# Kernel optimization log

Hardware: AMD Instinct MI355X
Metric: run time of the kernel (lower is better)

Reference implementation:

```python
import jax, jax.numpy as jnp
import numpy as np
from jax import lax

L, B, T = 512, 1024, 48


def setup_inputs() -> dict:
    key = jax.random.key(0)
    k1, k2, k3, k4, k5 = jax.random.split(key, 5)
    emissions = jax.random.normal(k1, (L, B, T), dtype=jnp.float32)
    tags = jax.random.randint(k2, (L, B), 0, T)
    mask = jnp.ones((L, B), dtype=bool)
    start_transitions = jax.random.uniform(k3, (T,), minval=-0.1, maxval=0.1, dtype=jnp.float32)
    end_transitions = jax.random.uniform(k4, (T,), minval=-0.1, maxval=0.1, dtype=jnp.float32)
    transitions = jax.random.uniform(k5, (T, T), minval=-0.1, maxval=0.1, dtype=jnp.float32)
    return {
        'emissions': emissions,
        'tags': tags,
        'mask': mask,
        'start_transitions': start_transitions,
        'end_transitions': end_transitions,
        'transitions': transitions,
    }


def reference(emissions, tags, mask, start_transitions, end_transitions, transitions):
    # emissions: [L, B, T] float; tags: [L, B] int; mask: [L, B] bool (seq-first)
    fm = mask.astype(emissions.dtype)
    seq_len, batch, _ = emissions.shape
    b_idx = jnp.arange(batch)

    # ---- numerator: score of the gold path ----
    # emission score at each step: emissions[i, b, tags[i, b]] -> [L, B]
    em_sc = jnp.take_along_axis(emissions, tags[:, :, None], axis=2)[:, :, 0]
    # transition score between consecutive tags -> [L-1, B]
    trans_sc = transitions[tags[:-1], tags[1:]]
    score = start_transitions[tags[0]] + em_sc[0]
    score = score + jnp.sum((trans_sc + em_sc[1:]) * fm[1:], axis=0)
    seq_ends = mask.astype(jnp.int32).sum(axis=0) - 1  # [B]
    last_tags = tags[seq_ends, b_idx]
    score = score + end_transitions[last_tags]

    # ---- denominator: log partition via forward algorithm (scan) ----
    alpha0 = start_transitions + emissions[0]  # [B, T]

    def step(alpha, xs):
        em, m = xs  # em: [B, T], m: [B]
        # [B, T(prev), T(next)] logsumexp over prev
        next_alpha = jax.nn.logsumexp(
            alpha[:, :, None] + transitions[None, :, :] + em[:, None, :], axis=1)
        alpha = jnp.where(m[:, None], next_alpha, alpha)
        return alpha, None

    alpha, _ = lax.scan(step, alpha0, (emissions[1:], mask[1:]))
    denominator = jax.nn.logsumexp(alpha + end_transitions, axis=1)  # [B]

    llh = score - denominator
    return jnp.mean(llh)  # reduction='mean' (default)
```

## Files before the change

kernel.cpp:

```cpp
#include <hip/hip_runtime.h>

#define LSEQ 512
#define BATCH 1024
#define T 48

__global__ __launch_bounds__(256) void crf_forward(
    const float* __restrict__ emissions,
    const int* __restrict__ mask,
    const float* __restrict__ start_tr,
    const float* __restrict__ end_tr,
    const float* __restrict__ trans,
    float* __restrict__ denom_out)
{
    const int wave = threadIdx.x >> 6;
    const int lane = threadIdx.x & 63;
    const int b    = blockIdx.x * 4 + wave;
    const int j    = lane;
    const bool valid = (j < T);
    const int jc   = valid ? j : (T - 1);

    float E_col[T];
    #pragma unroll
    for (int i = 0; i < T; ++i) {
        E_col[i] = __expf(trans[i * T + jc]);
    }

    float alpha = valid ? (start_tr[jc] + emissions[((size_t)0 * BATCH + b) * T + jc])
                        : -1e30f;

    float em_a = emissions[((size_t)1 * BATCH + b) * T + jc];
    float em_b = emissions[((size_t)2 * BATCH + b) * T + jc];
    int mk_a = mask[1 * BATCH + b];
    int mk_b = mask[2 * BATCH + b];

    for (int t = 1; t < LSEQ; ++t) {
        const float em_t = em_a;  em_a = em_b;
        const int mt = mk_a;  mk_a = mk_b;
        int tn = t + 2; if (tn > LSEQ - 1) tn = LSEQ - 1;
        em_b = emissions[((size_t)tn * BATCH + b) * T + jc];
        mk_b = mask[tn * BATCH + b];

        const float ref = __int_as_float(
            __builtin_amdgcn_readlane(__float_as_int(alpha), 0));
        const float p = __expf(alpha - ref);
        const int pbits = __float_as_int(p);

        float s0 = 0.f, s1 = 0.f, s2 = 0.f, s3 = 0.f;
        #pragma unroll
        for (int i = 0; i < T; i += 4) {
            s0 = __builtin_fmaf(__int_as_float(__builtin_amdgcn_readlane(pbits, i    )), E_col[i    ], s0);
            s1 = __builtin_fmaf(__int_as_float(__builtin_amdgcn_readlane(pbits, i + 1)), E_col[i + 1], s1);
            s2 = __builtin_fmaf(__int_as_float(__builtin_amdgcn_readlane(pbits, i + 2)), E_col[i + 2], s2);
            s3 = __builtin_fmaf(__int_as_float(__builtin_amdgcn_readlane(pbits, i + 3)), E_col[i + 3], s3);
        }
        const float s = (s0 + s1) + (s2 + s3);
        const float anew = em_t + ref + __logf(s);
        if (mt && valid) alpha = anew;
    }

    float v = valid ? (alpha + end_tr[jc]) : -1e30f;
    float m = v;
    #pragma unroll
    for (int off = 32; off > 0; off >>= 1) m = fmaxf(m, __shfl_xor(m, off));
    float e = __expf(v - m);
    #pragma unroll
    for (int off = 32; off > 0; off >>= 1) e += __shfl_xor(e, off);
    if (lane == 0) denom_out[b] = m + __logf(e);
}

__global__ __launch_bounds__(256) void crf_score_partial(
    const float* __restrict__ emissions,
    const int* __restrict__ tags,
    const int* __restrict__ mask,
    const float* __restrict__ trans,
    float* __restrict__ part,
    int* __restrict__ cnt)
{
    const int gid = blockIdx.x * blockDim.x + threadIdx.x;
    const int b = gid & (BATCH - 1);
    const int c = gid >> 10;
    const int t0 = c * 64;
    const int t1 = t0 + 64;

    float sc = 0.f;
    int ct = 0;
    const int tstart = (t0 == 0) ? 1 : t0;
    if (t0 == 0) ct += mask[b] ? 1 : 0;

    int tag_prev = tags[(tstart - 1) * BATCH + b];
    for (int t = tstart; t < t1; ++t) {
        const int tag = tags[t * BATCH + b];
        const int mt = mask[t * BATCH + b];
        if (mt) {
            sc += trans[tag_prev * T + tag]
                + emissions[((size_t)t * BATCH + b) * T + tag];
            ct += 1;
        }
        tag_prev = tag;
    }
    part[gid] = sc;
    cnt[gid] = ct;
}

__global__ __launch_bounds__(1024) void crf_combine(
    const float* __restrict__ emissions,
    const int* __restrict__ tags,
    const float* __restrict__ start_tr,
    const float* __restrict__ end_tr,
    const float* __restrict__ part,
    const int* __restrict__ cnt,
    const float* __restrict__ denom,
    float* __restrict__ out)
{
    const int b = threadIdx.x;

    const int tag0 = tags[b];
    float sc = start_tr[tag0] + emissions[(size_t)b * T + tag0];
    int ct = 0;
    #pragma unroll
    for (int c = 0; c < 8; ++c) {
        sc += part[c * BATCH + b];
        ct += cnt[c * BATCH + b];
    }
    if (ct < 1) ct = 1;
    const int last_tag = tags[(ct - 1) * BATCH + b];
    sc += end_tr[last_tag];

    const float llh = sc - denom[b];

    __shared__ float red[1024];
    red[b] = llh;
    __syncthreads();
    #pragma unroll
    for (int s = 512; s > 0; s >>= 1) {
        if (b < s) red[b] += red[b + s];
        __syncthreads();
    }
    if (b == 0) out[0] = red[0] / (float)BATCH;
}

extern "C" void kernel_launch(void* const* d_in, const int* in_sizes, int n_in,
                              void* d_out, int out_size, void* d_ws, size_t ws_size,
                              hipStream_t stream) {
    const float* emissions        = (const float*)d_in[0];
    const int* tags               = (const int*)d_in[1];
    const int* mask               = (const int*)d_in[2];
    const float* start_tr         = (const float*)d_in[3];
    const float* end_tr           = (const float*)d_in[4];
    const float* trans            = (const float*)d_in[5];
    float* out                    = (float*)d_out;

    float* denom = (float*)d_ws;
    float* part  = denom + BATCH;
    int*   cnt   = (int*)(part + 8 * BATCH);

    crf_forward<<<256, 256, 0, stream>>>(emissions, mask, start_tr, end_tr, trans, denom);
    crf_score_partial<<<32, 256, 0, stream>>>(emissions, tags, mask, trans, part, cnt);
    crf_combine<<<1, 1024, 0, stream>>>(emissions, tags, start_tr, end_tr,
                                        part, cnt, denom, out);
}
```

Measured before the change: 206.9 us.

## Rework forward recursion in linear space with packed fp16 dot2 and wider score split

The forward scan now keeps alpha in scaled linear form: a per-wave log scale C plus per-lane weights w. Each step needs one exp of the emission difference instead of an exp of alpha, and the recurrence is renormalized by lane 0's sum. The transition matrix and broadcast weights are packed into fp16 pairs so the inner product uses v_dot2 with half as many readlanes. The gold-path score kernel is also split into up to 32 time chunks when the workspace allows, for more parallelism. The fp16 weights and transitions lose precision, and anchoring the renormalization on lane 0 could overflow or underflow if lane 0's weight drifts far from the others.

```diff
diff --git a/kernel.cpp b/kernel.cpp
--- a/kernel.cpp
+++ b/kernel.cpp
@@ -4,7 +4,36 @@
 #define BATCH 1024
 #define T 48
 
-__global__ __launch_bounds__(256) void crf_forward(
+typedef __fp16 h2_t __attribute__((ext_vector_type(2)));
+
+static __device__ __forceinline__ float bcast_lane0(float x) {
+    return __int_as_float(__builtin_amdgcn_readfirstlane(__float_as_int(x)));
+}
+
+static __device__ __forceinline__ float dot2acc(int pk_bits, h2_t e, float acc) {
+#if __has_builtin(__builtin_amdgcn_fdot2)
+    return __builtin_amdgcn_fdot2(__builtin_bit_cast(h2_t, pk_bits), e, acc, false);
+#else
+    h2_t a = __builtin_bit_cast(h2_t, pk_bits);
+    return __builtin_fmaf((float)a.x, (float)e.x,
+           __builtin_fmaf((float)a.y, (float)e.y, acc));
+#endif
+}
+
+static __device__ __forceinline__ float fast_rcp(float x) {
+#if __has_builtin(__builtin_amdgcn_rcpf)
+    return __builtin_amdgcn_rcpf(x);
+#else
+    return 1.0f / x;
+#endif
+}
+
+static __device__ __forceinline__ int pack_pairs(float w) {
+    int wsh = __builtin_amdgcn_update_dpp(0, __float_as_int(w), 0x111, 0xF, 0xF, true);
+    return __builtin_bit_cast(int, __builtin_amdgcn_cvt_pkrtz(w, __int_as_float(wsh)));
+}
+
+__global__ __launch_bounds__(256, 1) void crf_forward(
     const float* __restrict__ emissions,
     const int* __restrict__ mask,
     const float* __restrict__ start_tr,
@@ -15,57 +44,67 @@
     const int wave = threadIdx.x >> 6;
     const int lane = threadIdx.x & 63;
     const int b    = blockIdx.x * 4 + wave;
-    const int j    = lane;
-    const bool valid = (j < T);
-    const int jc   = valid ? j : (T - 1);
-
-    float E_col[T];
+    const bool valid = (lane < T);
+    const int jc   = valid ? lane : (T - 1);
+
+    h2_t Ep[T / 2];
     #pragma unroll
-    for (int i = 0; i < T; ++i) {
-        E_col[i] = __expf(trans[i * T + jc]);
-    }
-
-    float alpha = valid ? (start_tr[jc] + emissions[((size_t)0 * BATCH + b) * T + jc])
-                        : -1e30f;
-
-    float em_a = emissions[((size_t)1 * BATCH + b) * T + jc];
-    float em_b = emissions[((size_t)2 * BATCH + b) * T + jc];
-    int mk_a = mask[1 * BATCH + b];
-    int mk_b = mask[2 * BATCH + b];
-
-    for (int t = 1; t < LSEQ; ++t) {
-        const float em_t = em_a;  em_a = em_b;
-        const int mt = mk_a;  mk_a = mk_b;
-        int tn = t + 2; if (tn > LSEQ - 1) tn = LSEQ - 1;
-        em_b = emissions[((size_t)tn * BATCH + b) * T + jc];
-        mk_b = mask[tn * BATCH + b];
-
-        const float ref = __int_as_float(
-            __builtin_amdgcn_readlane(__float_as_int(alpha), 0));
-        const float p = __expf(alpha - ref);
-        const int pbits = __float_as_int(p);
-
-        float s0 = 0.f, s1 = 0.f, s2 = 0.f, s3 = 0.f;
+    for (int k = 0; k < T / 2; ++k) {
+        float e0 = __expf(trans[(2 * k) * T + jc]);
+        float e1 = __expf(trans[(2 * k + 1) * T + jc]);
+        Ep[k] = __builtin_amdgcn_cvt_pkrtz(e0, e1);
+    }
+
+    const float a0 = start_tr[jc] + emissions[(size_t)b * T + jc];
+    const float A0 = bcast_lane0(a0);
+    float w = valid ? __expf(a0 - A0) : 0.f;
+    float C = A0;
+    int pk = pack_pairs(w);
+
+    float em0_ = emissions[((size_t)1 * BATCH + b) * T + jc];
+    float em1_ = emissions[((size_t)2 * BATCH + b) * T + jc];
+    float em2_ = emissions[((size_t)3 * BATCH + b) * T + jc];
+    float em3_ = emissions[((size_t)4 * BATCH + b) * T + jc];
+    int   mk0_ = mask[1 * BATCH + b];
+    int   mk1_ = mask[2 * BATCH + b];
+    int   mk2_ = mask[3 * BATCH + b];
+    int   mk3_ = mask[4 * BATCH + b];
+
+    for (int t = 1; t <= LSEQ - 1; ++t) {
+        const float em = em0_;  em0_ = em1_; em1_ = em2_; em2_ = em3_;
+        const int   mk = mk0_;  mk0_ = mk1_; mk1_ = mk2_; mk2_ = mk3_;
+        int tn = t + 4; if (tn > LSEQ - 1) tn = LSEQ - 1;
+        em3_ = emissions[((size_t)tn * BATCH + b) * T + jc];
+        mk3_ = mask[tn * BATCH + b];
+
+        const float em0 = bcast_lane0(em);
+        const float e   = __expf(em - em0);
+
+        float acc0 = 0.f, acc1 = 0.f, acc2 = 0.f, acc3 = 0.f;
         #pragma unroll
-        for (int i = 0; i < T; i += 4) {
-            s0 = __builtin_fmaf(__int_as_float(__builtin_amdgcn_readlane(pbits, i    )), E_col[i    ], s0);
-            s1 = __builtin_fmaf(__int_as_float(__builtin_amdgcn_readlane(pbits, i + 1)), E_col[i + 1], s1);
-            s2 = __builtin_fmaf(__int_as_float(__builtin_amdgcn_readlane(pbits, i + 2)), E_col[i + 2], s2);
-            s3 = __builtin_fmaf(__int_as_float(__builtin_amdgcn_readlane(pbits, i + 3)), E_col[i + 3], s3);
+        for (int k = 0; k < T / 2; k += 4) {
+            acc0 = dot2acc(__builtin_amdgcn_readlane(pk, 2 * k + 0), Ep[k + 0], acc0);
+            acc1 = dot2acc(__builtin_amdgcn_readlane(pk, 2 * k + 2), Ep[k + 1], acc1);
+            acc2 = dot2acc(__builtin_amdgcn_readlane(pk, 2 * k + 4), Ep[k + 2], acc2);
+            acc3 = dot2acc(__builtin_amdgcn_readlane(pk, 2 * k + 6), Ep[k + 3], acc3);
         }
-        const float s = (s0 + s1) + (s2 + s3);
-        const float anew = em_t + ref + __logf(s);
-        if (mt && valid) alpha = anew;
-    }
-
-    float v = valid ? (alpha + end_tr[jc]) : -1e30f;
-    float m = v;
+        const float S  = (acc0 + acc1) + (acc2 + acc3);
+        const float S0 = bcast_lane0(S);
+        const float rs = fast_rcp(S0);
+        const float lg = __logf(S0);
+        const float wnew = (e * rs) * S;
+
+        const bool upd = (mk != 0);
+        w = (upd && valid) ? wnew : w;
+        C = upd ? (C + em0 + lg) : C;
+
+        pk = pack_pairs(w);
+    }
+
+    float v = valid ? (w * __expf(end_tr[jc])) : 0.f;
     #pragma unroll
-    for (int off = 32; off > 0; off >>= 1) m = fmaxf(m, __shfl_xor(m, off));
-    float e = __expf(v - m);
-    #pragma unroll
-    for (int off = 32; off > 0; off >>= 1) e += __shfl_xor(e, off);
-    if (lane == 0) denom_out[b] = m + __logf(e);
+    for (int off = 32; off > 0; off >>= 1) v += __shfl_xor(v, off);
+    if (lane == 0) denom_out[b] = C + __logf(v);
 }
 
 __global__ __launch_bounds__(256) void crf_score_partial(
@@ -74,13 +113,14 @@
     const int* __restrict__ mask,
     const float* __restrict__ trans,
     float* __restrict__ part,
-    int* __restrict__ cnt)
+    int* __restrict__ cnt,
+    int csz)
 {
     const int gid = blockIdx.x * blockDim.x + threadIdx.x;
     const int b = gid & (BATCH - 1);
     const int c = gid >> 10;
-    const int t0 = c * 64;
-    const int t1 = t0 + 64;
+    const int t0 = c * csz;
+    const int t1 = t0 + csz;
 
     float sc = 0.f;
     int ct = 0;
@@ -110,15 +150,15 @@
     const float* __restrict__ part,
     const int* __restrict__ cnt,
     const float* __restrict__ denom,
-    float* __restrict__ out)
+    float* __restrict__ out,
+    int nchunk)
 {
     const int b = threadIdx.x;
 
     const int tag0 = tags[b];
     float sc = start_tr[tag0] + emissions[(size_t)b * T + tag0];
     int ct = 0;
-    #pragma unroll
-    for (int c = 0; c < 8; ++c) {
+    for (int c = 0; c < nchunk; ++c) {
         sc += part[c * BATCH + b];
         ct += cnt[c * BATCH + b];
     }
@@ -150,12 +190,16 @@
     const float* trans            = (const float*)d_in[5];
     float* out                    = (float*)d_out;
 
+    const int nchunk = (ws_size >= (size_t)(BATCH * 4 + 32 * BATCH * 8 + 64)) ? 32 : 8;
+    const int csz    = LSEQ / nchunk;
+
     float* denom = (float*)d_ws;
     float* part  = denom + BATCH;
-    int*   cnt   = (int*)(part + 8 * BATCH);
+    int*   cnt   = (int*)(part + nchunk * BATCH);
 
     crf_forward<<<256, 256, 0, stream>>>(emissions, mask, start_tr, end_tr, trans, denom);
-    crf_score_partial<<<32, 256, 0, stream>>>(emissions, tags, mask, trans, part, cnt);
+    crf_score_partial<<<nchunk * BATCH / 256, 256, 0, stream>>>(
+        emissions, tags, mask, trans, part, cnt, csz);
     crf_combine<<<1, 1024, 0, stream>>>(emissions, tags, start_tr, end_tr,
-                                        part, cnt, denom, out);
-}
+                                        part, cnt, denom, out, nchunk);
+}
```

Result: faster. 198.0 us (-4.3%).
